# Optimization experiments

Hardware: AMD Instinct MI355X
Metric: run time of the kernel (lower is better)

Reference implementation:

```python
import jax, jax.numpy as jnp
import numpy as np

NU = 200000  # num_users
NI = 200000  # num_items
D = 128      # d_model
B = 4096     # interaction batch


def setup_inputs() -> dict:
    key = jax.random.key(0)
    ks = jax.random.split(key, 24)
    f = lambda k, s, sc=1.0: (jax.random.normal(k, s, dtype=jnp.float32) * sc)
    s = 1.0 / np.sqrt(D)
    return {
        "user_id": jax.random.randint(ks[0], (B,), 0, NU),
        "prev_item_id": jax.random.randint(ks[1], (B,), 0, NI),
        "item_id": jax.random.randint(ks[2], (B,), 0, NI),
        "time_since_prev_item": jax.random.uniform(ks[3], (B, 1), dtype=jnp.float32),
        "time_since_prev_user": jax.random.uniform(ks[4], (B, 1), dtype=jnp.float32),
        "dynamic_user_emb": f(ks[5], (NU, D), 0.1),
        "dynamic_item_emb": f(ks[6], (NI, D), 0.1),
        "is_user_new": jnp.ones((NU, 1), dtype=jnp.float32),
        "is_item_new": jnp.ones((NI, 1), dtype=jnp.float32),
        "static_user_W": f(ks[7], (NU, D)),
        "static_item_W": f(ks[8], (NI, D)),
        "initial_user_emb": f(ks[9], (1, D)),
        "initial_item_emb": f(ks[10], (1, D)),
        "user_Wih": f(ks[11], (D, D + 1), s),
        "user_Whh": f(ks[12], (D, D), s),
        "user_bih": f(ks[13], (D,), s),
        "user_bhh": f(ks[14], (D,), s),
        "item_Wih": f(ks[15], (D, D + 1), s),
        "item_Whh": f(ks[16], (D, D), s),
        "item_bih": f(ks[17], (D,), s),
        "item_bhh": f(ks[18], (D,), s),
        "pred_W": f(ks[19], (2 * D, 4 * D), 1.0 / np.sqrt(4 * D)),
        "pred_b": f(ks[20], (2 * D,), 1.0 / np.sqrt(4 * D)),
        "td_W": f(ks[21], (D, 1)),
        "td_b": f(ks[22], (D,)),
    }


def _rnn_cell(x, h, Wih, Whh, bih, bhh):
    # torch.nn.RNNCell: tanh(x @ Wih^T + bih + h @ Whh^T + bhh)
    return jnp.tanh(x @ Wih.T + bih + h @ Whh.T + bhh)


def reference(user_id, prev_item_id, item_id, time_since_prev_item, time_since_prev_user,
              dynamic_user_emb, dynamic_item_emb, is_user_new, is_item_new,
              static_user_W, static_item_W, initial_user_emb, initial_item_emb,
              user_Wih, user_Whh, user_bih, user_bhh,
              item_Wih, item_Whh, item_bih, item_bhh,
              pred_W, pred_b, td_W, td_b):
    # gather dynamic embeddings (fall back to initial emb for new entities)
    user_emb = is_user_new[user_id] * initial_user_emb + dynamic_user_emb[user_id]
    item_emb = is_item_new[item_id] * initial_item_emb + dynamic_item_emb[item_id]
    prev_item_emb = is_item_new[prev_item_id] * initial_item_emb + dynamic_item_emb[prev_item_id]
    static_user_emb = static_user_W[user_id]
    static_item_emb = static_item_W[item_id]
    prev_static_item_emb = static_item_W[prev_item_id]

    # time projection + prediction head
    user_proj = user_emb * (1.0 + time_since_prev_item @ td_W.T + td_b)
    item_pred = jnp.concatenate(
        [user_proj, prev_item_emb, prev_static_item_emb, static_user_emb], axis=1) @ pred_W.T + pred_b
    item_target = jnp.concatenate([item_emb, static_item_emb], axis=1)

    # RNNCell updates
    updated_user_emb = _rnn_cell(jnp.concatenate([item_emb, time_since_prev_item], axis=1),
                                 user_emb, user_Wih, user_Whh, user_bih, user_bhh)
    updated_item_emb = _rnn_cell(jnp.concatenate([user_emb, time_since_prev_user], axis=1),
                                 item_emb, item_Wih, item_Whh, item_bih, item_bhh)

    # scatter back into persistent buffers (detached, as in torch)
    new_dyn_user = dynamic_user_emb.at[user_id].set(jax.lax.stop_gradient(updated_user_emb))
    new_dyn_item = dynamic_item_emb.at[item_id].set(jax.lax.stop_gradient(updated_item_emb))
    new_is_user_new = is_user_new.at[user_id].set(0.0)
    new_is_item_new = is_item_new.at[item_id].set(0.0)

    return (item_pred, item_target, updated_user_emb, user_emb, updated_item_emb, item_emb,
            new_dyn_user, new_dyn_item, new_is_user_new, new_is_item_new)
```

## Files before the change

### kernel.cpp

```cpp
#include <hip/hip_runtime.h>
#include <hip/hip_bf16.h>

#define NU 200000
#define NI 200000
#define D 128
#define BATCH 4096

typedef __bf16 bf16x8 __attribute__((ext_vector_type(8)));
typedef float f32x4 __attribute__((ext_vector_type(4)));

__device__ __forceinline__ void store_bf16x4(__hip_bfloat16* p, float4 v) {
    union { __hip_bfloat16 h[4]; uint2 u; } pk;
    pk.h[0] = __float2bfloat16(v.x);
    pk.h[1] = __float2bfloat16(v.y);
    pk.h[2] = __float2bfloat16(v.z);
    pk.h[3] = __float2bfloat16(v.w);
    *reinterpret_cast<uint2*>(p) = pk.u;
}

__device__ __forceinline__ float4 f4_fma(float s, float4 a, float4 b) {
    return make_float4(fmaf(s, a.x, b.x), fmaf(s, a.y, b.y),
                       fmaf(s, a.z, b.z), fmaf(s, a.w, b.w));
}

__global__ __launch_bounds__(256) void prep_gather_kernel(
    const int* __restrict__ uid, const int* __restrict__ pid,
    const int* __restrict__ iid,
    const float* __restrict__ t_i, const float* __restrict__ t_u,
    const float* __restrict__ dynU, const float* __restrict__ dynI,
    const float* __restrict__ isU, const float* __restrict__ isI,
    const float* __restrict__ statU, const float* __restrict__ statI,
    const float* __restrict__ initU, const float* __restrict__ initI,
    const float* __restrict__ tdW, const float* __restrict__ tdb,
    const float* __restrict__ predW,
    const float* __restrict__ uWih, const float* __restrict__ uWhh,
    const float* __restrict__ iWih, const float* __restrict__ iWhh,
    const float* __restrict__ ubih, const float* __restrict__ ubhh,
    const float* __restrict__ ibih, const float* __restrict__ ibhh,
    float* __restrict__ o_user_emb, float* __restrict__ o_item_emb,
    float* __restrict__ o_target,
    __hip_bfloat16* __restrict__ xpred,
    __hip_bfloat16* __restrict__ xhU, __hip_bfloat16* __restrict__ xhI,
    __hip_bfloat16* __restrict__ wPred,
    __hip_bfloat16* __restrict__ wU, __hip_bfloat16* __restrict__ wI,
    float* __restrict__ biasU, float* __restrict__ biasI,
    int* __restrict__ lastU, int* __restrict__ lastI)
{
    int idx = blockIdx.x * 256 + threadIdx.x;
    if (idx < 131072) {
        int b = idx >> 5;
        int g = idx & 31;
        const float4* dU4 = (const float4*)dynU;
        const float4* dI4 = (const float4*)dynI;
        const float4* sU4 = (const float4*)statU;
        const float4* sI4 = (const float4*)statI;

        int u = uid[b], i = iid[b], p = pid[b];
        float fu = isU[u], fi = isI[i], fp = isI[p];
        float ti = t_i[b], tu = t_u[b];

        float4 iu = ((const float4*)initU)[g];
        float4 ii = ((const float4*)initI)[g];
        float4 ue = f4_fma(fu, iu, dU4[(size_t)u * 32 + g]);
        float4 ie = f4_fma(fi, ii, dI4[(size_t)i * 32 + g]);
        float4 pe = f4_fma(fp, ii, dI4[(size_t)p * 32 + g]);
        float4 su = sU4[(size_t)u * 32 + g];
        float4 si = sI4[(size_t)i * 32 + g];
        float4 sp = sI4[(size_t)p * 32 + g];
        float4 tw = ((const float4*)tdW)[g];
        float4 tb = ((const float4*)tdb)[g];

        ((float4*)o_user_emb)[(size_t)b * 32 + g] = ue;
        ((float4*)o_item_emb)[(size_t)b * 32 + g] = ie;
        ((float4*)o_target)[(size_t)b * 64 + g] = ie;
        ((float4*)o_target)[(size_t)b * 64 + 32 + g] = si;

        float4 f = f4_fma(ti, tw, tb);
        float4 proj = make_float4(ue.x * (1.0f + f.x), ue.y * (1.0f + f.y),
                                  ue.z * (1.0f + f.z), ue.w * (1.0f + f.w));

        __hip_bfloat16* xp = xpred + (size_t)b * 512;
        store_bf16x4(xp + 4 * g, proj);
        store_bf16x4(xp + 128 + 4 * g, pe);
        store_bf16x4(xp + 256 + 4 * g, sp);
        store_bf16x4(xp + 384 + 4 * g, su);

        __hip_bfloat16* xu = xhU + (size_t)b * 288;
        store_bf16x4(xu + 4 * g, ue);
        store_bf16x4(xu + 128 + 4 * g, ie);
        __hip_bfloat16* xi = xhI + (size_t)b * 288;
        store_bf16x4(xi + 4 * g, ie);
        store_bf16x4(xi + 128 + 4 * g, ue);
        if (g < 8) {
            float4 zu = make_float4(g == 0 ? ti : 0.0f, 0.0f, 0.0f, 0.0f);
            float4 zi = make_float4(g == 0 ? tu : 0.0f, 0.0f, 0.0f, 0.0f);
            store_bf16x4(xu + 256 + 4 * g, zu);
            store_bf16x4(xi + 256 + 4 * g, zi);
        }
        return;
    }
    idx -= 131072;
    if (idx < 131072) {
        wPred[idx] = __float2bfloat16(predW[idx]);
        return;
    }
    idx -= 131072;
    if (idx < 73728) {
        int z = idx / 36864;
        int r = idx - z * 36864;
        int j = r / 288, k = r - (r / 288) * 288;
        const float* Wih = z ? iWih : uWih;
        const float* Whh = z ? iWhh : uWhh;
        float v = 0.0f;
        if (k < 128)      v = Whh[j * 128 + k];
        else if (k < 257) v = Wih[j * 129 + (k - 128)];
        __hip_bfloat16* W = z ? wI : wU;
        W[j * 288 + k] = __float2bfloat16(v);
        return;
    }
    idx -= 73728;
    if (idx < 128) { biasU[idx] = ubih[idx] + ubhh[idx]; return; }
    idx -= 128;
    if (idx < 128) { biasI[idx] = ibih[idx] + ibhh[idx]; return; }
    idx -= 128;
    if (idx < BATCH) { atomicMax(&lastU[uid[idx]], idx); return; }
    idx -= BATCH;
    if (idx < BATCH) { atomicMax(&lastI[iid[idx]], idx); return; }
}

__global__ __launch_bounds__(256) void gemm_copy_kernel(
    const __hip_bfloat16* __restrict__ xpred,
    const __hip_bfloat16* __restrict__ wPred,
    const float* __restrict__ predb, float* __restrict__ o_pred,
    const __hip_bfloat16* __restrict__ xhU, const __hip_bfloat16* __restrict__ xhI,
    const __hip_bfloat16* __restrict__ wU, const __hip_bfloat16* __restrict__ wI,
    const float* __restrict__ biasU, const float* __restrict__ biasI,
    const int* __restrict__ uid, const int* __restrict__ iid,
    const int* __restrict__ lastU, const int* __restrict__ lastI,
    float* __restrict__ o_updU, float* __restrict__ o_updI,
    float* __restrict__ o_dynU, float* __restrict__ o_dynI,
    const float* __restrict__ dynU, const float* __restrict__ dynI,
    const float* __restrict__ isU, const float* __restrict__ isI,
    float* __restrict__ o_isU, float* __restrict__ o_isI)
{
    int bx = blockIdx.x;
    int tid = threadIdx.x;

    if (bx >= 512) {
        int idx = (bx - 512) * 256 + tid;
        if (idx < 6400000) {
            int row = idx >> 5;
            if (lastU[row] < 0) {
                f32x4 v = __builtin_nontemporal_load((const f32x4*)dynU + idx);
                __builtin_nontemporal_store(v, (f32x4*)o_dynU + idx);
            }
            return;
        }
        idx -= 6400000;
        if (idx < 6400000) {
            int row = idx >> 5;
            if (lastI[row] < 0) {
                f32x4 v = __builtin_nontemporal_load((const f32x4*)dynI + idx);
                __builtin_nontemporal_store(v, (f32x4*)o_dynI + idx);
            }
            return;
        }
        idx -= 6400000;
        if (idx < 50000) {
            int4 l = ((const int4*)lastU)[idx];
            float4 v = ((const float4*)isU)[idx];
            float4 o = make_float4(l.x >= 0 ? 0.0f : v.x,
                                   l.y >= 0 ? 0.0f : v.y,
                                   l.z >= 0 ? 0.0f : v.z,
                                   l.w >= 0 ? 0.0f : v.w);
            ((float4*)o_isU)[idx] = o;
            return;
        }
        idx -= 50000;
        if (idx < 50000) {
            int4 l = ((const int4*)lastI)[idx];
            float4 v = ((const float4*)isI)[idx];
            float4 o = make_float4(l.x >= 0 ? 0.0f : v.x,
                                   l.y >= 0 ? 0.0f : v.y,
                                   l.z >= 0 ? 0.0f : v.z,
                                   l.w >= 0 ? 0.0f : v.w);
            ((float4*)o_isI)[idx] = o;
            return;
        }
        return;
    }

    int wave = tid >> 6, lane = tid & 63, quad = lane >> 4, l15 = lane & 15;

    if (bx < 256) {
        const int K = 512;
        int m0 = (bx & 63) * 64, n0 = (bx >> 6) * 64;
        f32x4 acc[4] = {};
        const __hip_bfloat16* Arow = xpred + (size_t)(m0 + wave * 16 + l15) * K;
        for (int k0 = 0; k0 < K; k0 += 32) {
            bf16x8 a = *reinterpret_cast<const bf16x8*>(Arow + k0 + quad * 8);
#pragma unroll
            for (int ct = 0; ct < 4; ++ct) {
                bf16x8 b = *reinterpret_cast<const bf16x8*>(
                    wPred + (size_t)(n0 + ct * 16 + l15) * K + k0 + quad * 8);
                acc[ct] = __builtin_amdgcn_mfma_f32_16x16x32_bf16(a, b, acc[ct], 0, 0, 0);
            }
        }
        int orow = m0 + wave * 16 + quad * 4;
#pragma unroll
        for (int ct = 0; ct < 4; ++ct) {
            int col = n0 + ct * 16 + l15;
            float bc = predb[col];
#pragma unroll
            for (int r = 0; r < 4; ++r)
                o_pred[(size_t)(orow + r) * 256 + col] = acc[ct][r] + bc;
        }
    } else {
        bx -= 256;
        int z = bx >> 7; bx &= 127;
        int m0 = (bx & 63) * 64, n0 = (bx >> 6) * 64;
        const __hip_bfloat16* A = z ? xhI : xhU;
        const __hip_bfloat16* W = z ? wI : wU;
        const float* bias = z ? biasI : biasU;
        const int* ids  = z ? iid : uid;
        const int* last = z ? lastI : lastU;
        float* outB = z ? o_updI : o_updU;
        float* outD = z ? o_dynI : o_dynU;

        const int K = 288;
        f32x4 acc[4] = {};
        const __hip_bfloat16* Arow = A + (size_t)(m0 + wave * 16 + l15) * K;
        for (int k0 = 0; k0 < K; k0 += 32) {
            bf16x8 a = *reinterpret_cast<const bf16x8*>(Arow + k0 + quad * 8);
#pragma unroll
            for (int ct = 0; ct < 4; ++ct) {
                bf16x8 b = *reinterpret_cast<const bf16x8*>(
                    W + (size_t)(n0 + ct * 16 + l15) * K + k0 + quad * 8);
                acc[ct] = __builtin_amdgcn_mfma_f32_16x16x32_bf16(a, b, acc[ct], 0, 0, 0);
            }
        }
        int orow = m0 + wave * 16 + quad * 4;
        int rid[4], win[4];
#pragma unroll
        for (int r = 0; r < 4; ++r) {
            int row = orow + r;
            rid[r] = ids[row];
            win[r] = (last[rid[r]] == row);
        }
#pragma unroll
        for (int ct = 0; ct < 4; ++ct) {
            int col = n0 + ct * 16 + l15;
            float bc = bias[col];
#pragma unroll
            for (int r = 0; r < 4; ++r) {
                float v = tanhf(acc[ct][r] + bc);
                outB[(size_t)(orow + r) * D + col] = v;
                if (win[r]) outD[(size_t)rid[r] * D + col] = v;
            }
        }
    }
}

extern "C" void kernel_launch(void* const* d_in, const int* in_sizes, int n_in,
                              void* d_out, int out_size, void* d_ws, size_t ws_size,
                              hipStream_t stream) {
    const int*   uid   = (const int*)d_in[0];
    const int*   pid   = (const int*)d_in[1];
    const int*   iid   = (const int*)d_in[2];
    const float* t_i   = (const float*)d_in[3];
    const float* t_u   = (const float*)d_in[4];
    const float* dynU  = (const float*)d_in[5];
    const float* dynI  = (const float*)d_in[6];
    const float* isU   = (const float*)d_in[7];
    const float* isI   = (const float*)d_in[8];
    const float* statU = (const float*)d_in[9];
    const float* statI = (const float*)d_in[10];
    const float* initU = (const float*)d_in[11];
    const float* initI = (const float*)d_in[12];
    const float* uWih  = (const float*)d_in[13];
    const float* uWhh  = (const float*)d_in[14];
    const float* ubih  = (const float*)d_in[15];
    const float* ubhh  = (const float*)d_in[16];
    const float* iWih  = (const float*)d_in[17];
    const float* iWhh  = (const float*)d_in[18];
    const float* ibih  = (const float*)d_in[19];
    const float* ibhh  = (const float*)d_in[20];
    const float* predW = (const float*)d_in[21];
    const float* predb = (const float*)d_in[22];
    const float* tdW   = (const float*)d_in[23];
    const float* tdb   = (const float*)d_in[24];

    float* out = (float*)d_out;
    float* o_pred     = out;
    float* o_target   = out + 1048576;
    float* o_updU     = out + 2097152;
    float* o_userEmb  = out + 2621440;
    float* o_updI     = out + 3145728;
    float* o_itemEmb  = out + 3670016;
    float* o_dynU     = out + 4194304;
    float* o_dynI     = out + 29794304;
    float* o_isU      = out + 55394304;
    float* o_isI      = out + 55594304;

    char* ws = (char*)d_ws;
    int* lastU = (int*)ws;
    int* lastI = lastU + NU;
    __hip_bfloat16* xpred = (__hip_bfloat16*)(ws + 1600000);
    __hip_bfloat16* xhU   = (__hip_bfloat16*)(ws + 5794304);
    __hip_bfloat16* xhI   = (__hip_bfloat16*)(ws + 8153600);
    __hip_bfloat16* wPred = (__hip_bfloat16*)(ws + 10512896);
    __hip_bfloat16* wU    = (__hip_bfloat16*)(ws + 10775040);
    __hip_bfloat16* wI    = (__hip_bfloat16*)(ws + 10848768);
    float* biasU = (float*)(ws + 10922496);
    float* biasI = (float*)(ws + 10923008);

    hipMemsetAsync(lastU, 0xFF, (size_t)(NU + NI) * sizeof(int), stream);

    prep_gather_kernel<<<1345, 256, 0, stream>>>(
        uid, pid, iid, t_i, t_u, dynU, dynI, isU, isI, statU, statI,
        initU, initI, tdW, tdb,
        predW, uWih, uWhh, iWih, iWhh, ubih, ubhh, ibih, ibhh,
        o_userEmb, o_itemEmb, o_target, xpred, xhU, xhI,
        wPred, wU, wI, biasU, biasI, lastU, lastI);

    gemm_copy_kernel<<<50903, 256, 0, stream>>>(
        xpred, wPred, predb, o_pred,
        xhU, xhI, wU, wI, biasU, biasI,
        uid, iid, lastU, lastI,
        o_updU, o_updI, o_dynU, o_dynI,
        dynU, dynI, isU, isI, o_isU, o_isI);
}
```

Measured before the change: 505.0 us.

## Fuse embedding gather into GEMM A-fragment loads, drop bf16 staging buffers

Moves the per-row gather and blend of dynamic, static and initial embeddings out of the prep kernel and into the GEMM blocks, which now build bf16 A fragments in registers straight from the fp32 tables. This removes the round trip through the xpred, xhU and xhI bf16 workspace buffers. The fp32 embedding and target outputs are written by a separate block range inside the same mega kernel, so the prep kernel shrinks to weight conversion and the last-writer atomics. The dyn-table copy also switches from nontemporal to plain loads and stores. In exchange, each N-tile block re-gathers the same rows, adding redundant global reads, and the 16-entry fragment array raises register pressure.

```diff
diff --git a/kernel.cpp b/kernel.cpp
--- a/kernel.cpp
+++ b/kernel.cpp
@@ -8,6 +8,20 @@
 
 typedef __bf16 bf16x8 __attribute__((ext_vector_type(8)));
 typedef float f32x4 __attribute__((ext_vector_type(4)));
+struct f8 { f32x4 lo, hi; };
+
+__device__ __forceinline__ f8 ld8(const float* p) {
+    f8 r; r.lo = *(const f32x4*)p; r.hi = *(const f32x4*)(p + 4); return r;
+}
+
+__device__ __forceinline__ bf16x8 cvt8(f8 v) {
+    union { __hip_bfloat16 h[8]; bf16x8 b; } u;
+    u.h[0] = __float2bfloat16(v.lo.x); u.h[1] = __float2bfloat16(v.lo.y);
+    u.h[2] = __float2bfloat16(v.lo.z); u.h[3] = __float2bfloat16(v.lo.w);
+    u.h[4] = __float2bfloat16(v.hi.x); u.h[5] = __float2bfloat16(v.hi.y);
+    u.h[6] = __float2bfloat16(v.hi.z); u.h[7] = __float2bfloat16(v.hi.w);
+    return u.b;
+}
 
 __device__ __forceinline__ void store_bf16x4(__hip_bfloat16* p, float4 v) {
     union { __hip_bfloat16 h[4]; uint2 u; } pk;
@@ -23,83 +37,19 @@
                        fmaf(s, a.z, b.z), fmaf(s, a.w, b.w));
 }
 
-__global__ __launch_bounds__(256) void prep_gather_kernel(
-    const int* __restrict__ uid, const int* __restrict__ pid,
-    const int* __restrict__ iid,
-    const float* __restrict__ t_i, const float* __restrict__ t_u,
-    const float* __restrict__ dynU, const float* __restrict__ dynI,
-    const float* __restrict__ isU, const float* __restrict__ isI,
-    const float* __restrict__ statU, const float* __restrict__ statI,
-    const float* __restrict__ initU, const float* __restrict__ initI,
-    const float* __restrict__ tdW, const float* __restrict__ tdb,
+__global__ __launch_bounds__(256) void prep_kernel(
     const float* __restrict__ predW,
     const float* __restrict__ uWih, const float* __restrict__ uWhh,
     const float* __restrict__ iWih, const float* __restrict__ iWhh,
     const float* __restrict__ ubih, const float* __restrict__ ubhh,
     const float* __restrict__ ibih, const float* __restrict__ ibhh,
-    float* __restrict__ o_user_emb, float* __restrict__ o_item_emb,
-    float* __restrict__ o_target,
-    __hip_bfloat16* __restrict__ xpred,
-    __hip_bfloat16* __restrict__ xhU, __hip_bfloat16* __restrict__ xhI,
+    const int* __restrict__ uid, const int* __restrict__ iid,
     __hip_bfloat16* __restrict__ wPred,
     __hip_bfloat16* __restrict__ wU, __hip_bfloat16* __restrict__ wI,
     float* __restrict__ biasU, float* __restrict__ biasI,
     int* __restrict__ lastU, int* __restrict__ lastI)
 {
     int idx = blockIdx.x * 256 + threadIdx.x;
-    if (idx < 131072) {
-        int b = idx >> 5;
-        int g = idx & 31;
-        const float4* dU4 = (const float4*)dynU;
-        const float4* dI4 = (const float4*)dynI;
-        const float4* sU4 = (const float4*)statU;
-        const float4* sI4 = (const float4*)statI;
-
-        int u = uid[b], i = iid[b], p = pid[b];
-        float fu = isU[u], fi = isI[i], fp = isI[p];
-        float ti = t_i[b], tu = t_u[b];
-
-        float4 iu = ((const float4*)initU)[g];
-        float4 ii = ((const float4*)initI)[g];
-        float4 ue = f4_fma(fu, iu, dU4[(size_t)u * 32 + g]);
-        float4 ie = f4_fma(fi, ii, dI4[(size_t)i * 32 + g]);
-        float4 pe = f4_fma(fp, ii, dI4[(size_t)p * 32 + g]);
-        float4 su = sU4[(size_t)u * 32 + g];
-        float4 si = sI4[(size_t)i * 32 + g];
-        float4 sp = sI4[(size_t)p * 32 + g];
-        float4 tw = ((const float4*)tdW)[g];
-        float4 tb = ((const float4*)tdb)[g];
-
-        ((float4*)o_user_emb)[(size_t)b * 32 + g] = ue;
-        ((float4*)o_item_emb)[(size_t)b * 32 + g] = ie;
-        ((float4*)o_target)[(size_t)b * 64 + g] = ie;
-        ((float4*)o_target)[(size_t)b * 64 + 32 + g] = si;
-
-        float4 f = f4_fma(ti, tw, tb);
-        float4 proj = make_float4(ue.x * (1.0f + f.x), ue.y * (1.0f + f.y),
-                                  ue.z * (1.0f + f.z), ue.w * (1.0f + f.w));
-
-        __hip_bfloat16* xp = xpred + (size_t)b * 512;
-        store_bf16x4(xp + 4 * g, proj);
-        store_bf16x4(xp + 128 + 4 * g, pe);
-        store_bf16x4(xp + 256 + 4 * g, sp);
-        store_bf16x4(xp + 384 + 4 * g, su);
-
-        __hip_bfloat16* xu = xhU + (size_t)b * 288;
-        store_bf16x4(xu + 4 * g, ue);
-        store_bf16x4(xu + 128 + 4 * g, ie);
-        __hip_bfloat16* xi = xhI + (size_t)b * 288;
-        store_bf16x4(xi + 4 * g, ie);
-        store_bf16x4(xi + 128 + 4 * g, ue);
-        if (g < 8) {
-            float4 zu = make_float4(g == 0 ? ti : 0.0f, 0.0f, 0.0f, 0.0f);
-            float4 zi = make_float4(g == 0 ? tu : 0.0f, 0.0f, 0.0f, 0.0f);
-            store_bf16x4(xu + 256 + 4 * g, zu);
-            store_bf16x4(xi + 256 + 4 * g, zi);
-        }
-        return;
-    }
-    idx -= 131072;
     if (idx < 131072) {
         wPred[idx] = __float2bfloat16(predW[idx]);
         return;
@@ -128,82 +78,128 @@
     if (idx < BATCH) { atomicMax(&lastI[iid[idx]], idx); return; }
 }
 
-__global__ __launch_bounds__(256) void gemm_copy_kernel(
-    const __hip_bfloat16* __restrict__ xpred,
-    const __hip_bfloat16* __restrict__ wPred,
-    const float* __restrict__ predb, float* __restrict__ o_pred,
-    const __hip_bfloat16* __restrict__ xhU, const __hip_bfloat16* __restrict__ xhI,
+__global__ __launch_bounds__(256) void mega_kernel(
+    const int* __restrict__ uid, const int* __restrict__ pid,
+    const int* __restrict__ iid,
+    const float* __restrict__ t_i, const float* __restrict__ t_u,
+    const float* __restrict__ dynU, const float* __restrict__ dynI,
+    const float* __restrict__ isU, const float* __restrict__ isI,
+    const float* __restrict__ statU, const float* __restrict__ statI,
+    const float* __restrict__ initU, const float* __restrict__ initI,
+    const float* __restrict__ tdW, const float* __restrict__ tdb,
+    const __hip_bfloat16* __restrict__ wPred, const float* __restrict__ predb,
     const __hip_bfloat16* __restrict__ wU, const __hip_bfloat16* __restrict__ wI,
     const float* __restrict__ biasU, const float* __restrict__ biasI,
-    const int* __restrict__ uid, const int* __restrict__ iid,
     const int* __restrict__ lastU, const int* __restrict__ lastI,
+    float* __restrict__ o_pred,
     float* __restrict__ o_updU, float* __restrict__ o_updI,
+    float* __restrict__ o_userEmb, float* __restrict__ o_itemEmb,
+    float* __restrict__ o_target,
     float* __restrict__ o_dynU, float* __restrict__ o_dynI,
-    const float* __restrict__ dynU, const float* __restrict__ dynI,
-    const float* __restrict__ isU, const float* __restrict__ isI,
     float* __restrict__ o_isU, float* __restrict__ o_isI)
 {
     int bx = blockIdx.x;
     int tid = threadIdx.x;
 
-    if (bx >= 512) {
-        int idx = (bx - 512) * 256 + tid;
+    if (bx >= 1024) {
+        int idx = (bx - 1024) * 256 + tid;
         if (idx < 6400000) {
-            int row = idx >> 5;
-            if (lastU[row] < 0) {
-                f32x4 v = __builtin_nontemporal_load((const f32x4*)dynU + idx);
-                __builtin_nontemporal_store(v, (f32x4*)o_dynU + idx);
-            }
+            if (lastU[idx >> 5] < 0)
+                ((float4*)o_dynU)[idx] = ((const float4*)dynU)[idx];
             return;
         }
         idx -= 6400000;
         if (idx < 6400000) {
-            int row = idx >> 5;
-            if (lastI[row] < 0) {
-                f32x4 v = __builtin_nontemporal_load((const f32x4*)dynI + idx);
-                __builtin_nontemporal_store(v, (f32x4*)o_dynI + idx);
-            }
+            if (lastI[idx >> 5] < 0)
+                ((float4*)o_dynI)[idx] = ((const float4*)dynI)[idx];
             return;
         }
         idx -= 6400000;
         if (idx < 50000) {
             int4 l = ((const int4*)lastU)[idx];
             float4 v = ((const float4*)isU)[idx];
-            float4 o = make_float4(l.x >= 0 ? 0.0f : v.x,
-                                   l.y >= 0 ? 0.0f : v.y,
-                                   l.z >= 0 ? 0.0f : v.z,
-                                   l.w >= 0 ? 0.0f : v.w);
-            ((float4*)o_isU)[idx] = o;
+            ((float4*)o_isU)[idx] = make_float4(l.x >= 0 ? 0.0f : v.x,
+                                                l.y >= 0 ? 0.0f : v.y,
+                                                l.z >= 0 ? 0.0f : v.z,
+                                                l.w >= 0 ? 0.0f : v.w);
             return;
         }
         idx -= 50000;
         if (idx < 50000) {
             int4 l = ((const int4*)lastI)[idx];
             float4 v = ((const float4*)isI)[idx];
-            float4 o = make_float4(l.x >= 0 ? 0.0f : v.x,
-                                   l.y >= 0 ? 0.0f : v.y,
-                                   l.z >= 0 ? 0.0f : v.z,
-                                   l.w >= 0 ? 0.0f : v.w);
-            ((float4*)o_isI)[idx] = o;
+            ((float4*)o_isI)[idx] = make_float4(l.x >= 0 ? 0.0f : v.x,
+                                                l.y >= 0 ? 0.0f : v.y,
+                                                l.z >= 0 ? 0.0f : v.z,
+                                                l.w >= 0 ? 0.0f : v.w);
             return;
         }
         return;
     }
 
+    if (bx >= 512) {
+        int idx = (bx - 512) * 256 + tid;
+        int b = idx >> 5, g = idx & 31;
+        const float4* dU4 = (const float4*)dynU;
+        const float4* dI4 = (const float4*)dynI;
+        const float4* sI4 = (const float4*)statI;
+        int u = uid[b], i = iid[b];
+        float fu = isU[u], fi = isI[i];
+        float4 iu = ((const float4*)initU)[g];
+        float4 ii = ((const float4*)initI)[g];
+        float4 ue = f4_fma(fu, iu, dU4[(size_t)u * 32 + g]);
+        float4 ie = f4_fma(fi, ii, dI4[(size_t)i * 32 + g]);
+        float4 si = sI4[(size_t)i * 32 + g];
+        ((float4*)o_userEmb)[(size_t)b * 32 + g] = ue;
+        ((float4*)o_itemEmb)[(size_t)b * 32 + g] = ie;
+        ((float4*)o_target)[(size_t)b * 64 + g] = ie;
+        ((float4*)o_target)[(size_t)b * 64 + 32 + g] = si;
+        return;
+    }
+
     int wave = tid >> 6, lane = tid & 63, quad = lane >> 4, l15 = lane & 15;
 
     if (bx < 256) {
+        int m0 = (bx & 63) * 64, n0 = (bx >> 6) * 64;
+        int rowb = m0 + wave * 16 + l15;
+        int u = uid[rowb], p = pid[rowb];
+        float fu = isU[u], fp = isI[p], ti = t_i[rowb];
+
+        bf16x8 afr[16];
+#pragma unroll
+        for (int kk = 0; kk < 16; ++kk) {
+            int off = (kk & 3) * 32 + quad * 8;
+            f8 x;
+            if ((kk >> 2) == 0) {
+                f8 du = ld8(dynU + (size_t)u * 128 + off);
+                f8 iu = ld8(initU + off);
+                f8 tw = ld8(tdW + off);
+                f8 tb = ld8(tdb + off);
+                x.lo = (fu * iu.lo + du.lo) * (1.0f + (ti * tw.lo + tb.lo));
+                x.hi = (fu * iu.hi + du.hi) * (1.0f + (ti * tw.hi + tb.hi));
+            } else if ((kk >> 2) == 1) {
+                f8 dp = ld8(dynI + (size_t)p * 128 + off);
+                f8 ii = ld8(initI + off);
+                x.lo = fp * ii.lo + dp.lo;
+                x.hi = fp * ii.hi + dp.hi;
+            } else if ((kk >> 2) == 2) {
+                x = ld8(statI + (size_t)p * 128 + off);
+            } else {
+                x = ld8(statU + (size_t)u * 128 + off);
+            }
+            afr[kk] = cvt8(x);
+        }
+
         const int K = 512;
-        int m0 = (bx & 63) * 64, n0 = (bx >> 6) * 64;
         f32x4 acc[4] = {};
-        const __hip_bfloat16* Arow = xpred + (size_t)(m0 + wave * 16 + l15) * K;
-        for (int k0 = 0; k0 < K; k0 += 32) {
-            bf16x8 a = *reinterpret_cast<const bf16x8*>(Arow + k0 + quad * 8);
+#pragma unroll
+        for (int kk = 0; kk < 16; ++kk) {
+            int k0 = kk * 32;
 #pragma unroll
             for (int ct = 0; ct < 4; ++ct) {
                 bf16x8 b = *reinterpret_cast<const bf16x8*>(
                     wPred + (size_t)(n0 + ct * 16 + l15) * K + k0 + quad * 8);
-                acc[ct] = __builtin_amdgcn_mfma_f32_16x16x32_bf16(a, b, acc[ct], 0, 0, 0);
+                acc[ct] = __builtin_amdgcn_mfma_f32_16x16x32_bf16(afr[kk], b, acc[ct], 0, 0, 0);
             }
         }
         int orow = m0 + wave * 16 + quad * 4;
@@ -216,10 +212,9 @@
                 o_pred[(size_t)(orow + r) * 256 + col] = acc[ct][r] + bc;
         }
     } else {
-        bx -= 256;
-        int z = bx >> 7; bx &= 127;
-        int m0 = (bx & 63) * 64, n0 = (bx >> 6) * 64;
-        const __hip_bfloat16* A = z ? xhI : xhU;
+        int bz = bx - 256;
+        int z = bz >> 7; bz &= 127;
+        int m0 = (bz & 63) * 64, n0 = (bz >> 6) * 64;
         const __hip_bfloat16* W = z ? wI : wU;
         const float* bias = z ? biasI : biasU;
         const int* ids  = z ? iid : uid;
@@ -227,16 +222,46 @@
         float* outB = z ? o_updI : o_updU;
         float* outD = z ? o_dynI : o_dynU;
 
+        int rowb = m0 + wave * 16 + l15;
+        int u = uid[rowb], i = iid[rowb];
+        float fu = isU[u], fi = isI[i];
+        float tt = z ? t_u[rowb] : t_i[rowb];
+
+        bf16x8 afr[9];
+#pragma unroll
+        for (int kk = 0; kk < 9; ++kk) {
+            int off = (kk & 3) * 32 + quad * 8;
+            f8 x;
+            if (kk < 8) {
+                bool want_ue = (kk < 4) ^ (z != 0);
+                if (want_ue) {
+                    f8 du = ld8(dynU + (size_t)u * 128 + off);
+                    f8 iu = ld8(initU + off);
+                    x.lo = fu * iu.lo + du.lo;
+                    x.hi = fu * iu.hi + du.hi;
+                } else {
+                    f8 di = ld8(dynI + (size_t)i * 128 + off);
+                    f8 ii = ld8(initI + off);
+                    x.lo = fi * ii.lo + di.lo;
+                    x.hi = fi * ii.hi + di.hi;
+                }
+            } else {
+                x.lo = 0.0f; x.hi = 0.0f;
+                if (quad == 0) x.lo.x = tt;
+            }
+            afr[kk] = cvt8(x);
+        }
+
         const int K = 288;
         f32x4 acc[4] = {};
-        const __hip_bfloat16* Arow = A + (size_t)(m0 + wave * 16 + l15) * K;
-        for (int k0 = 0; k0 < K; k0 += 32) {
-            bf16x8 a = *reinterpret_cast<const bf16x8*>(Arow + k0 + quad * 8);
+#pragma unroll
+        for (int kk = 0; kk < 9; ++kk) {
+            int k0 = kk * 32;
 #pragma unroll
             for (int ct = 0; ct < 4; ++ct) {
                 bf16x8 b = *reinterpret_cast<const bf16x8*>(
                     W + (size_t)(n0 + ct * 16 + l15) * K + k0 + quad * 8);
-                acc[ct] = __builtin_amdgcn_mfma_f32_16x16x32_bf16(a, b, acc[ct], 0, 0, 0);
+                acc[ct] = __builtin_amdgcn_mfma_f32_16x16x32_bf16(afr[kk], b, acc[ct], 0, 0, 0);
             }
         }
         int orow = m0 + wave * 16 + quad * 4;
@@ -305,9 +330,6 @@
     char* ws = (char*)d_ws;
     int* lastU = (int*)ws;
     int* lastI = lastU + NU;
-    __hip_bfloat16* xpred = (__hip_bfloat16*)(ws + 1600000);
-    __hip_bfloat16* xhU   = (__hip_bfloat16*)(ws + 5794304);
-    __hip_bfloat16* xhI   = (__hip_bfloat16*)(ws + 8153600);
     __hip_bfloat16* wPred = (__hip_bfloat16*)(ws + 10512896);
     __hip_bfloat16* wU    = (__hip_bfloat16*)(ws + 10775040);
     __hip_bfloat16* wI    = (__hip_bfloat16*)(ws + 10848768);
@@ -316,17 +338,14 @@
 
     hipMemsetAsync(lastU, 0xFF, (size_t)(NU + NI) * sizeof(int), stream);
 
-    prep_gather_kernel<<<1345, 256, 0, stream>>>(
+    prep_kernel<<<833, 256, 0, stream>>>(
+        predW, uWih, uWhh, iWih, iWhh, ubih, ubhh, ibih, ibhh,
+        uid, iid, wPred, wU, wI, biasU, biasI, lastU, lastI);
+
+    mega_kernel<<<51415, 256, 0, stream>>>(
         uid, pid, iid, t_i, t_u, dynU, dynI, isU, isI, statU, statI,
         initU, initI, tdW, tdb,
-        predW, uWih, uWhh, iWih, iWhh, ubih, ubhh, ibih, ibhh,
-        o_userEmb, o_itemEmb, o_target, xpred, xhU, xhI,
-        wPred, wU, wI, biasU, biasI, lastU, lastI);
-
-    gemm_copy_kernel<<<50903, 256, 0, stream>>>(
-        xpred, wPred, predb, o_pred,
-        xhU, xhI, wU, wI, biasU, biasI,
-        uid, iid, lastU, lastI,
-        o_updU, o_updI, o_dynU, o_dynI,
-        dynU, dynI, isU, isI, o_isU, o_isI);
-}
+        wPred, predb, wU, wI, biasU, biasI, lastU, lastI,
+        o_pred, o_updU, o_updI, o_userEmb, o_itemEmb, o_target,
+        o_dynU, o_dynI, o_isU, o_isI);
+}
```

Result: slower. 517.2 us (+2.4%).
